# Kernel tuning notes

Hardware: AMD Instinct MI355X
Metric: run time of the kernel (lower is better)

Reference implementation:

```python
import jax, jax.numpy as jnp
import numpy as np

D_MODEL = 1024
N_HEADS = 16
HEAD_DIM = D_MODEL // N_HEADS


def setup_inputs() -> dict:
    key = jax.random.key(0)
    ks = jax.random.split(key, 10)
    B, NQ, S = 8, 64, 4096
    inv = 1.0 / np.sqrt(D_MODEL)
    inp = {
        "queries": jax.random.normal(ks[0], (B, NQ, D_MODEL), dtype=jnp.float32),
        "context": jax.random.normal(ks[1], (B, S, D_MODEL), dtype=jnp.float32),
        "wq": jax.random.normal(ks[2], (D_MODEL, D_MODEL), dtype=jnp.float32) * inv,
        "bq": jnp.zeros((D_MODEL,), dtype=jnp.float32),
        "wk": jax.random.normal(ks[3], (D_MODEL, D_MODEL), dtype=jnp.float32) * inv,
        "bk": jnp.zeros((D_MODEL,), dtype=jnp.float32),
        "wv": jax.random.normal(ks[4], (D_MODEL, D_MODEL), dtype=jnp.float32) * inv,
        "bv": jnp.zeros((D_MODEL,), dtype=jnp.float32),
        "wo": jax.random.normal(ks[5], (D_MODEL, D_MODEL), dtype=jnp.float32) * inv,
        "bo": jnp.zeros((D_MODEL,), dtype=jnp.float32),
    }
    return inp


def reference(queries, context, wq, bq, wk, bk, wv, bv, wo, bo):
    B, NQ, D = queries.shape
    S = context.shape[1]
    H, HD = N_HEADS, HEAD_DIM
    scale = HD ** -0.5
    # projections (x @ W^T + b, matching nn.Linear)
    q = queries @ wq.T + bq            # (B, NQ, D)
    k = context @ wk.T + bk            # (B, S, D)
    v = context @ wv.T + bv            # (B, S, D)
    q = q.reshape(B, NQ, H, HD).transpose(0, 2, 1, 3)  # (B, H, NQ, HD)
    k = k.reshape(B, S, H, HD).transpose(0, 2, 1, 3)   # (B, H, S, HD)
    v = v.reshape(B, S, H, HD).transpose(0, 2, 1, 3)   # (B, H, S, HD)
    attn = jnp.einsum('bhnd,bhsd->bhns', q, k) * scale
    attn = jax.nn.softmax(attn, axis=-1)
    # dropout is identity at eval / p=0
    out = jnp.einsum('bhns,bhsd->bhnd', attn, v)        # (B, H, NQ, HD)
    out = out.transpose(0, 2, 1, 3).reshape(B, NQ, D)   # (B, NQ, D)
    return out @ wo.T + bo
```

## Files before the change

kernel.cpp:

```cpp
#include <hip/hip_runtime.h>
#include <stdint.h>

#define BATCH   8
#define NQL     64
#define SLEN    4096
#define DMODEL  1024
#define NHEADS  16
#define HDIM    64

typedef float          f32x4  __attribute__((ext_vector_type(4)));
typedef __bf16         bf16x8 __attribute__((ext_vector_type(8)));
typedef unsigned int   u32x4  __attribute__((ext_vector_type(4)));
typedef unsigned short u16x4  __attribute__((ext_vector_type(4)));
typedef unsigned short u16x8  __attribute__((ext_vector_type(8)));

__device__ __forceinline__ unsigned short f2bf(float f) {
  unsigned int u = __builtin_bit_cast(unsigned int, f);
  u += 0x7FFFu + ((u >> 16) & 1u);
  return (unsigned short)(u >> 16);
}

__device__ __forceinline__ f32x4 mfma16(bf16x8 a, bf16x8 b, f32x4 c) {
  return __builtin_amdgcn_mfma_f32_16x16x32_bf16(a, b, c, 0, 0, 0);
}

__device__ __forceinline__ bf16x8 lds_frag(const char* p) {
  u32x4 v = *(const u32x4*)p;
  return __builtin_bit_cast(bf16x8, v);
}

__device__ __forceinline__ void gload_lds16(const void* g, void* l) {
  __builtin_amdgcn_global_load_lds((const __attribute__((address_space(1))) void*)g,
                                   (__attribute__((address_space(3))) void*)l, 16, 0, 0);
}

__global__ __launch_bounds__(256) void cvt_bf16_kernel(const float* __restrict__ in,
                                                       unsigned short* __restrict__ out,
                                                       int n8) {
  int i = blockIdx.x * 256 + threadIdx.x;
  if (i >= n8) return;
  const float4* p = (const float4*)in + (size_t)i * 2;
  float4 a = p[0], b = p[1];
  u16x8 o;
  o[0] = f2bf(a.x); o[1] = f2bf(a.y); o[2] = f2bf(a.z); o[3] = f2bf(a.w);
  o[4] = f2bf(b.x); o[5] = f2bf(b.y); o[6] = f2bf(b.z); o[7] = f2bf(b.w);
  *((u16x8*)out + i) = o;
}

template<int MODE>
__global__ __launch_bounds__(256)
void gemm_bt(const unsigned short* __restrict__ A, const unsigned short* __restrict__ Bw,
             const float* __restrict__ bias, void* __restrict__ Cout,
             int M, int N, int K) {
  __shared__ char lds[32768];
  char* ldsA = lds;
  char* ldsB = lds + 16384;

  const int tid  = threadIdx.x;
  const int wave = tid >> 6, lane = tid & 63;
  const int g    = lane >> 4, ln = lane & 15;
  const int nbn  = N >> 7;
  const int brow = (int)(blockIdx.x / nbn) << 7;
  const int bcol = (int)(blockIdx.x % nbn) << 7;
  const int wr   = wave >> 1, wc = wave & 1;

  f32x4 acc[4][4];
#pragma unroll
  for (int i = 0; i < 4; ++i)
#pragma unroll
    for (int j = 0; j < 4; ++j) acc[i][j] = (f32x4){0.f, 0.f, 0.f, 0.f};

  const int KT = K >> 6;
  const int srow = lane >> 3;
  const int srcs = (lane & 7) ^ (srow & 7);

  for (int kt = 0; kt < KT; ++kt) {
#pragma unroll
    for (int c = wave; c < 16; c += 4) {
      int row = (c << 3) + srow;
      const char* ga = (const char*)A + (((size_t)(brow + row) * K + (kt << 6) + (srcs << 3)) << 1);
      gload_lds16(ga, ldsA + (c << 10));
      const char* gb = (const char*)Bw + (((size_t)(bcol + row) * K + (kt << 6) + (srcs << 3)) << 1);
      gload_lds16(gb, ldsB + (c << 10));
    }
    asm volatile("s_waitcnt vmcnt(0)" ::: "memory");
    __syncthreads();

#pragma unroll
    for (int ks = 0; ks < 2; ++ks) {
      bf16x8 af[4], bfr[4];
      const int slot = ((ks << 2) + g) ^ (ln & 7);
#pragma unroll
      for (int mt = 0; mt < 4; ++mt) {
        int row = wr * 64 + mt * 16 + ln;
        af[mt] = lds_frag(ldsA + row * 128 + (slot << 4));
      }
#pragma unroll
      for (int nt = 0; nt < 4; ++nt) {
        int row = wc * 64 + nt * 16 + ln;
        bfr[nt] = lds_frag(ldsB + row * 128 + (slot << 4));
      }
#pragma unroll
      for (int mt = 0; mt < 4; ++mt)
#pragma unroll
        for (int nt = 0; nt < 4; ++nt)
          acc[mt][nt] = mfma16(af[mt], bfr[nt], acc[mt][nt]);
    }
    __syncthreads();
  }

#pragma unroll
  for (int mt = 0; mt < 4; ++mt) {
#pragma unroll
    for (int nt = 0; nt < 4; ++nt) {
      f32x4 v = acc[mt][nt];
      int r0 = brow + wr * 64 + mt * 16 + g * 4;
      int c  = bcol + wc * 64 + nt * 16 + ln;
      float bi = bias[c];
      if constexpr (MODE == 0) {
        unsigned short* Cb = (unsigned short*)Cout;
#pragma unroll
        for (int j = 0; j < 4; ++j) Cb[(size_t)(r0 + j) * N + c] = f2bf(v[j] + bi);
      } else if constexpr (MODE == 1) {
        float* Cf = (float*)Cout;
#pragma unroll
        for (int j = 0; j < 4; ++j) Cf[(size_t)(r0 + j) * N + c] = v[j] + bi;
      } else {
        u16x4 pk;
#pragma unroll
        for (int j = 0; j < 4; ++j) pk[j] = f2bf(v[j] + bi);
        size_t base = ((size_t)(r0 >> 12) * 1024 + c) * 4096 + (size_t)(r0 & 4095);
        *(u16x4*)((unsigned short*)Cout + base) = pk;
      }
    }
  }
}

__global__ __launch_bounds__(256)
void attn_kernel(const unsigned short* __restrict__ Qp,
                 const unsigned short* __restrict__ Kp,
                 const unsigned short* __restrict__ Vt,
                 unsigned short* __restrict__ Aout) {
  __shared__ char ldsKV[2][16384];
  __shared__ unsigned int plds[4 * 16 * 36];

  const int bh = blockIdx.x;
  const int b = bh >> 4, h = bh & 15;
  const int tid = threadIdx.x;
  const int wave = tid >> 6, lane = tid & 63;
  const int g = lane >> 4, ln = lane & 15;
  const int pbase = wave * 576 + ln * 36;
  const int srow = lane >> 3;
  const int srcs = (lane & 7) ^ (srow & 7);

  const unsigned short* qb =
      Qp + ((size_t)(b * 64 + wave * 16 + ln) * 1024) + h * 64 + g * 8;
  bf16x8 qf[2];
  qf[0] = __builtin_bit_cast(bf16x8, *(const u32x4*)qb);
  qf[1] = __builtin_bit_cast(bf16x8, *(const u32x4*)(qb + 32));

  f32x4 oacc[4];
#pragma unroll
  for (int i = 0; i < 4; ++i) oacc[i] = (f32x4){0.f, 0.f, 0.f, 0.f};
  float mrun = -1e30f, lrun = 0.f;

  auto stage = [&](int t, int buf) {
    int s0 = t << 6;
    char* bK = ldsKV[buf];
#pragma unroll
    for (int c4 = 0; c4 < 4; ++c4) {
      int c = wave * 4 + c4;
      int cc = c & 7;
      int row = (cc << 3) + srow;
      const char* gsrc;
      if (c < 8)
        gsrc = (const char*)Kp + (((size_t)((b << 12) + s0 + row) * 1024 + (h << 6) + (srcs << 3)) << 1);
      else
        gsrc = (const char*)Vt + (((size_t)((b << 10) + (h << 6) + row) * 4096 + s0 + (srcs << 3)) << 1);
      gload_lds16(gsrc, bK + ((c < 8) ? 0 : 8192) + (cc << 10));
    }
  };

  stage(0, 0);
  const int NT = SLEN / 64;
  for (int t = 0; t < NT; ++t) {
    asm volatile("s_waitcnt vmcnt(0)" ::: "memory");
    __syncthreads();
    if (t + 1 < NT) stage(t + 1, (t + 1) & 1);

    char* bufK = ldsKV[t & 1];
    char* bufV = bufK + 8192;

    f32x4 s4[4];
#pragma unroll
    for (int i = 0; i < 4; ++i) s4[i] = (f32x4){0.f, 0.f, 0.f, 0.f};
#pragma unroll
    for (int ks = 0; ks < 2; ++ks) {
      const int slot = ((ks << 2) + g) ^ (ln & 7);
#pragma unroll
      for (int mt = 0; mt < 4; ++mt) {
        int row = mt * 16 + ln;
        s4[mt] = mfma16(lds_frag(bufK + row * 128 + (slot << 4)), qf[ks], s4[mt]);
      }
    }

    float tmax = -1e30f;
#pragma unroll
    for (int mt = 0; mt < 4; ++mt)
#pragma unroll
      for (int j = 0; j < 4; ++j) {
        float sv = s4[mt][j] * 0.125f;
        s4[mt][j] = sv;
        tmax = fmaxf(tmax, sv);
      }
    tmax = fmaxf(tmax, __shfl_xor(tmax, 16));
    tmax = fmaxf(tmax, __shfl_xor(tmax, 32));
    float mnew = fmaxf(mrun, tmax);
    float factor = __expf(mrun - mnew);
    float psum = 0.f;
#pragma unroll
    for (int mt = 0; mt < 4; ++mt) {
      float p0 = __expf(s4[mt][0] - mnew);
      float p1 = __expf(s4[mt][1] - mnew);
      float p2 = __expf(s4[mt][2] - mnew);
      float p3 = __expf(s4[mt][3] - mnew);
      psum += (p0 + p1) + (p2 + p3);
      plds[pbase + mt * 8 + g * 2 + 0] = (unsigned)f2bf(p0) | ((unsigned)f2bf(p1) << 16);
      plds[pbase + mt * 8 + g * 2 + 1] = (unsigned)f2bf(p2) | ((unsigned)f2bf(p3) << 16);
    }
    psum += __shfl_xor(psum, 16);
    psum += __shfl_xor(psum, 32);
    lrun = lrun * factor + psum;
    mrun = mnew;

    float fj0 = __shfl(factor, g * 4 + 0);
    float fj1 = __shfl(factor, g * 4 + 1);
    float fj2 = __shfl(factor, g * 4 + 2);
    float fj3 = __shfl(factor, g * 4 + 3);
#pragma unroll
    for (int nt = 0; nt < 4; ++nt) {
      oacc[nt][0] *= fj0; oacc[nt][1] *= fj1; oacc[nt][2] *= fj2; oacc[nt][3] *= fj3;
    }

#pragma unroll
    for (int kt2 = 0; kt2 < 2; ++kt2) {
      u32x4 pv;
      int pidx = pbase + kt2 * 16 + g * 4;
      pv[0] = plds[pidx]; pv[1] = plds[pidx + 1]; pv[2] = plds[pidx + 2]; pv[3] = plds[pidx + 3];
      bf16x8 pa = __builtin_bit_cast(bf16x8, pv);
      const int slot = ((kt2 << 2) + g) ^ (ln & 7);
#pragma unroll
      for (int nt = 0; nt < 4; ++nt) {
        int row = nt * 16 + ln;
        oacc[nt] = mfma16(pa, lds_frag(bufV + row * 128 + (slot << 4)), oacc[nt]);
      }
    }
  }

  float l0 = __shfl(lrun, g * 4 + 0);
  float l1 = __shfl(lrun, g * 4 + 1);
  float l2 = __shfl(lrun, g * 4 + 2);
  float l3 = __shfl(lrun, g * 4 + 3);
  float r0 = 1.f / l0, r1 = 1.f / l1, r2 = 1.f / l2, r3 = 1.f / l3;
#pragma unroll
  for (int nt = 0; nt < 4; ++nt) {
    int col = h * 64 + nt * 16 + ln;
    size_t rbase = (size_t)(b * 64 + wave * 16 + g * 4) * 1024 + col;
    Aout[rbase + 0 * 1024] = f2bf(oacc[nt][0] * r0);
    Aout[rbase + 1 * 1024] = f2bf(oacc[nt][1] * r1);
    Aout[rbase + 2 * 1024] = f2bf(oacc[nt][2] * r2);
    Aout[rbase + 3 * 1024] = f2bf(oacc[nt][3] * r3);
  }
}

extern "C" void kernel_launch(void* const* d_in, const int* in_sizes, int n_in,
                              void* d_out, int out_size, void* d_ws, size_t ws_size,
                              hipStream_t stream) {
  const float* queries = (const float*)d_in[0];
  const float* context = (const float*)d_in[1];
  const float* wq = (const float*)d_in[2];
  const float* bq = (const float*)d_in[3];
  const float* wk = (const float*)d_in[4];
  const float* bk = (const float*)d_in[5];
  const float* wv = (const float*)d_in[6];
  const float* bv = (const float*)d_in[7];
  const float* wo = (const float*)d_in[8];
  const float* bo = (const float*)d_in[9];

  const size_t CTX_E = (size_t)BATCH * SLEN * DMODEL;
  const size_t QRY_E = (size_t)BATCH * NQL * DMODEL;
  const size_t W_E   = (size_t)DMODEL * DMODEL;

  char* ws = (char*)d_ws;
  size_t off = 0;
  auto alloc = [&](size_t bytes) {
    char* p = ws + off;
    off += (bytes + 255) & ~(size_t)255;
    return p;
  };
  unsigned short* ctx_bf = (unsigned short*)alloc(CTX_E * 2);
  unsigned short* q_bf   = (unsigned short*)alloc(QRY_E * 2);
  unsigned short* wq_bf  = (unsigned short*)alloc(W_E * 2);
  unsigned short* wk_bf  = (unsigned short*)alloc(W_E * 2);
  unsigned short* wv_bf  = (unsigned short*)alloc(W_E * 2);
  unsigned short* wo_bf  = (unsigned short*)alloc(W_E * 2);
  unsigned short* Qp     = (unsigned short*)alloc(QRY_E * 2);
  unsigned short* Kp     = (unsigned short*)alloc(CTX_E * 2);
  unsigned short* Vt     = (unsigned short*)alloc(CTX_E * 2);
  unsigned short* Ao     = (unsigned short*)alloc(QRY_E * 2);
  if (off > ws_size) return;

  cvt_bf16_kernel<<<dim3((int)(CTX_E / 8 / 256)), 256, 0, stream>>>(context, ctx_bf, (int)(CTX_E / 8));
  cvt_bf16_kernel<<<dim3((int)(QRY_E / 8 / 256)), 256, 0, stream>>>(queries, q_bf, (int)(QRY_E / 8));
  cvt_bf16_kernel<<<dim3((int)(W_E / 8 / 256)), 256, 0, stream>>>(wq, wq_bf, (int)(W_E / 8));
  cvt_bf16_kernel<<<dim3((int)(W_E / 8 / 256)), 256, 0, stream>>>(wk, wk_bf, (int)(W_E / 8));
  cvt_bf16_kernel<<<dim3((int)(W_E / 8 / 256)), 256, 0, stream>>>(wv, wv_bf, (int)(W_E / 8));
  cvt_bf16_kernel<<<dim3((int)(W_E / 8 / 256)), 256, 0, stream>>>(wo, wo_bf, (int)(W_E / 8));

  const int M_KV = BATCH * SLEN;
  const int M_Q  = BATCH * NQL;

  gemm_bt<0><<<dim3((M_KV / 128) * (DMODEL / 128)), 256, 0, stream>>>(ctx_bf, wk_bf, bk, Kp, M_KV, DMODEL, DMODEL);
  gemm_bt<2><<<dim3((M_KV / 128) * (DMODEL / 128)), 256, 0, stream>>>(ctx_bf, wv_bf, bv, Vt, M_KV, DMODEL, DMODEL);
  gemm_bt<0><<<dim3((M_Q / 128) * (DMODEL / 128)), 256, 0, stream>>>(q_bf, wq_bf, bq, Qp, M_Q, DMODEL, DMODEL);

  attn_kernel<<<dim3(BATCH * NHEADS), 256, 0, stream>>>(Qp, Kp, Vt, Ao);

  gemm_bt<1><<<dim3((M_Q / 128) * (DMODEL / 128)), 256, 0, stream>>>(Ao, wo_bf, bo, d_out, M_Q, DMODEL, DMODEL);
}
```

Measured before the change: 532.1 us.

## Split attention over sequence, double-buffer GEMM, fuse conversions, remap GEMM blocks

The sequence dimension of attention is split into 8 chunks, giving 1024 workgroups instead of 128, and a new combine kernel merges the partial softmax results. The GEMM moves from single-buffered to double-buffered LDS with a partial vmcnt wait and raises MFMA priority with s_setprio. It also remaps workgroup IDs across 8 XCDs. The six fp32-to-bf16 conversion launches are fused into one. This adds a combine launch plus extra fp32 partial-result traffic, and the partials reuse the ctx_bf buffer after the K/V GEMMs have finished with it.

```diff
diff --git a/kernel.cpp b/kernel.cpp
--- a/kernel.cpp
+++ b/kernel.cpp
@@ -7,6 +7,7 @@
 #define DMODEL  1024
 #define NHEADS  16
 #define HDIM    64
+#define NSPLIT  8
 
 typedef float          f32x4  __attribute__((ext_vector_type(4)));
 typedef __bf16         bf16x8 __attribute__((ext_vector_type(8)));
@@ -34,17 +35,27 @@
                                    (__attribute__((address_space(3))) void*)l, 16, 0, 0);
 }
 
-__global__ __launch_bounds__(256) void cvt_bf16_kernel(const float* __restrict__ in,
-                                                       unsigned short* __restrict__ out,
-                                                       int n8) {
+__global__ __launch_bounds__(256)
+void cvt6_kernel(const float* __restrict__ p0, const float* __restrict__ p1,
+                 const float* __restrict__ p2, const float* __restrict__ p3,
+                 const float* __restrict__ p4, const float* __restrict__ p5,
+                 unsigned short* __restrict__ o0, unsigned short* __restrict__ o1,
+                 unsigned short* __restrict__ o2, unsigned short* __restrict__ o3,
+                 unsigned short* __restrict__ o4, unsigned short* __restrict__ o5) {
   int i = blockIdx.x * 256 + threadIdx.x;
-  if (i >= n8) return;
-  const float4* p = (const float4*)in + (size_t)i * 2;
+  const float* src; unsigned short* dst; int rel;
+  if      (i < 4194304) { src = p0; dst = o0; rel = i; }
+  else if (i < 4259840) { src = p1; dst = o1; rel = i - 4194304; }
+  else if (i < 4390912) { src = p2; dst = o2; rel = i - 4259840; }
+  else if (i < 4521984) { src = p3; dst = o3; rel = i - 4390912; }
+  else if (i < 4653056) { src = p4; dst = o4; rel = i - 4521984; }
+  else                  { src = p5; dst = o5; rel = i - 4653056; }
+  const float4* p = (const float4*)src + (size_t)rel * 2;
   float4 a = p[0], b = p[1];
   u16x8 o;
   o[0] = f2bf(a.x); o[1] = f2bf(a.y); o[2] = f2bf(a.z); o[3] = f2bf(a.w);
   o[4] = f2bf(b.x); o[5] = f2bf(b.y); o[6] = f2bf(b.z); o[7] = f2bf(b.w);
-  *((u16x8*)out + i) = o;
+  *((u16x8*)dst + rel) = o;
 }
 
 template<int MODE>
@@ -52,16 +63,19 @@
 void gemm_bt(const unsigned short* __restrict__ A, const unsigned short* __restrict__ Bw,
              const float* __restrict__ bias, void* __restrict__ Cout,
              int M, int N, int K) {
-  __shared__ char lds[32768];
-  char* ldsA = lds;
-  char* ldsB = lds + 16384;
+  __shared__ char lds[65536];
 
   const int tid  = threadIdx.x;
   const int wave = tid >> 6, lane = tid & 63;
   const int g    = lane >> 4, ln = lane & 15;
+
+  const int nwg = (int)gridDim.x;
+  const int cpx = nwg >> 3;
+  const int bid = (int)blockIdx.x;
+  const int wg  = (bid & 7) * cpx + (bid >> 3);
   const int nbn  = N >> 7;
-  const int brow = (int)(blockIdx.x / nbn) << 7;
-  const int bcol = (int)(blockIdx.x % nbn) << 7;
+  const int brow = (wg / nbn) << 7;
+  const int bcol = (wg % nbn) << 7;
   const int wr   = wave >> 1, wc = wave & 1;
 
   f32x4 acc[4][4];
@@ -74,17 +88,28 @@
   const int srow = lane >> 3;
   const int srcs = (lane & 7) ^ (srow & 7);
 
-  for (int kt = 0; kt < KT; ++kt) {
+  auto stage = [&](int kt, char* buf) {
 #pragma unroll
     for (int c = wave; c < 16; c += 4) {
       int row = (c << 3) + srow;
       const char* ga = (const char*)A + (((size_t)(brow + row) * K + (kt << 6) + (srcs << 3)) << 1);
-      gload_lds16(ga, ldsA + (c << 10));
+      gload_lds16(ga, buf + (c << 10));
       const char* gb = (const char*)Bw + (((size_t)(bcol + row) * K + (kt << 6) + (srcs << 3)) << 1);
-      gload_lds16(gb, ldsB + (c << 10));
-    }
-    asm volatile("s_waitcnt vmcnt(0)" ::: "memory");
-    __syncthreads();
+      gload_lds16(gb, buf + 16384 + (c << 10));
+    }
+  };
+
+  stage(0, lds);
+  for (int kt = 0; kt < KT; ++kt) {
+    char* cur = lds + ((kt & 1) << 15);
+    if (kt + 1 < KT) {
+      stage(kt + 1, lds + (((kt + 1) & 1) << 15));
+      asm volatile("s_waitcnt vmcnt(8)" ::: "memory");
+    } else {
+      asm volatile("s_waitcnt vmcnt(0)" ::: "memory");
+    }
+    __builtin_amdgcn_s_barrier();
+    __builtin_amdgcn_sched_barrier(0);
 
 #pragma unroll
     for (int ks = 0; ks < 2; ++ks) {
@@ -93,20 +118,22 @@
 #pragma unroll
       for (int mt = 0; mt < 4; ++mt) {
         int row = wr * 64 + mt * 16 + ln;
-        af[mt] = lds_frag(ldsA + row * 128 + (slot << 4));
+        af[mt] = lds_frag(cur + row * 128 + (slot << 4));
       }
 #pragma unroll
       for (int nt = 0; nt < 4; ++nt) {
         int row = wc * 64 + nt * 16 + ln;
-        bfr[nt] = lds_frag(ldsB + row * 128 + (slot << 4));
-      }
+        bfr[nt] = lds_frag(cur + 16384 + row * 128 + (slot << 4));
+      }
+      __builtin_amdgcn_s_setprio(1);
 #pragma unroll
       for (int mt = 0; mt < 4; ++mt)
 #pragma unroll
         for (int nt = 0; nt < 4; ++nt)
           acc[mt][nt] = mfma16(af[mt], bfr[nt], acc[mt][nt]);
-    }
-    __syncthreads();
+      __builtin_amdgcn_s_setprio(0);
+    }
+    __builtin_amdgcn_s_barrier();
   }
 
 #pragma unroll
@@ -137,14 +164,17 @@
 }
 
 __global__ __launch_bounds__(256)
-void attn_kernel(const unsigned short* __restrict__ Qp,
-                 const unsigned short* __restrict__ Kp,
-                 const unsigned short* __restrict__ Vt,
-                 unsigned short* __restrict__ Aout) {
+void attn_split(const unsigned short* __restrict__ Qp,
+                const unsigned short* __restrict__ Kp,
+                const unsigned short* __restrict__ Vt,
+                float* __restrict__ Opart,
+                float* __restrict__ Mpart,
+                float* __restrict__ Lpart) {
   __shared__ char ldsKV[2][16384];
   __shared__ unsigned int plds[4 * 16 * 36];
 
-  const int bh = blockIdx.x;
+  const int bh = (int)blockIdx.x / NSPLIT;
+  const int sp = (int)blockIdx.x % NSPLIT;
   const int b = bh >> 4, h = bh & 15;
   const int tid = threadIdx.x;
   const int wave = tid >> 6, lane = tid & 63;
@@ -181,19 +211,21 @@
     }
   };
 
-  stage(0, 0);
-  const int NT = SLEN / 64;
-  for (int t = 0; t < NT; ++t) {
+  const int T0 = sp * (SLEN / 64 / NSPLIT);
+  const int NTL = SLEN / 64 / NSPLIT;
+  stage(T0, 0);
+  for (int tl = 0; tl < NTL; ++tl) {
     asm volatile("s_waitcnt vmcnt(0)" ::: "memory");
     __syncthreads();
-    if (t + 1 < NT) stage(t + 1, (t + 1) & 1);
-
-    char* bufK = ldsKV[t & 1];
+    if (tl + 1 < NTL) stage(T0 + tl + 1, (tl + 1) & 1);
+
+    char* bufK = ldsKV[tl & 1];
     char* bufV = bufK + 8192;
 
     f32x4 s4[4];
 #pragma unroll
     for (int i = 0; i < 4; ++i) s4[i] = (f32x4){0.f, 0.f, 0.f, 0.f};
+    __builtin_amdgcn_s_setprio(1);
 #pragma unroll
     for (int ks = 0; ks < 2; ++ks) {
       const int slot = ((ks << 2) + g) ^ (ln & 7);
@@ -203,6 +235,7 @@
         s4[mt] = mfma16(lds_frag(bufK + row * 128 + (slot << 4)), qf[ks], s4[mt]);
       }
     }
+    __builtin_amdgcn_s_setprio(0);
 
     float tmax = -1e30f;
 #pragma unroll
@@ -242,6 +275,7 @@
       oacc[nt][0] *= fj0; oacc[nt][1] *= fj1; oacc[nt][2] *= fj2; oacc[nt][3] *= fj3;
     }
 
+    __builtin_amdgcn_s_setprio(1);
 #pragma unroll
     for (int kt2 = 0; kt2 < 2; ++kt2) {
       u32x4 pv;
@@ -255,22 +289,49 @@
         oacc[nt] = mfma16(pa, lds_frag(bufV + row * 128 + (slot << 4)), oacc[nt]);
       }
     }
-  }
-
-  float l0 = __shfl(lrun, g * 4 + 0);
-  float l1 = __shfl(lrun, g * 4 + 1);
-  float l2 = __shfl(lrun, g * 4 + 2);
-  float l3 = __shfl(lrun, g * 4 + 3);
-  float r0 = 1.f / l0, r1 = 1.f / l1, r2 = 1.f / l2, r3 = 1.f / l3;
+    __builtin_amdgcn_s_setprio(0);
+  }
+
+  const int rowb = sp * (BATCH * NHEADS * 64) + bh * 64;
 #pragma unroll
   for (int nt = 0; nt < 4; ++nt) {
-    int col = h * 64 + nt * 16 + ln;
-    size_t rbase = (size_t)(b * 64 + wave * 16 + g * 4) * 1024 + col;
-    Aout[rbase + 0 * 1024] = f2bf(oacc[nt][0] * r0);
-    Aout[rbase + 1 * 1024] = f2bf(oacc[nt][1] * r1);
-    Aout[rbase + 2 * 1024] = f2bf(oacc[nt][2] * r2);
-    Aout[rbase + 3 * 1024] = f2bf(oacc[nt][3] * r3);
-  }
+#pragma unroll
+    for (int j = 0; j < 4; ++j) {
+      int q = wave * 16 + g * 4 + j;
+      Opart[(size_t)(rowb + q) * 64 + nt * 16 + ln] = oacc[nt][j];
+    }
+  }
+  if (g == 0) {
+    Mpart[rowb + wave * 16 + ln] = mrun;
+    Lpart[rowb + wave * 16 + ln] = lrun;
+  }
+}
+
+__global__ __launch_bounds__(256)
+void attn_combine(const float* __restrict__ Opart, const float* __restrict__ Mpart,
+                  const float* __restrict__ Lpart, unsigned short* __restrict__ Aout) {
+  const int blk = blockIdx.x;
+  const int bh = blk >> 4;
+  const int q  = ((blk & 15) << 2) + (threadIdx.x >> 6);
+  const int hd = threadIdx.x & 63;
+  const int row = bh * 64 + q;
+
+  float mi[NSPLIT];
+  float M = -1e30f;
+#pragma unroll
+  for (int i = 0; i < NSPLIT; ++i) {
+    mi[i] = Mpart[i * 8192 + row];
+    M = fmaxf(M, mi[i]);
+  }
+  float L = 0.f, o = 0.f;
+#pragma unroll
+  for (int i = 0; i < NSPLIT; ++i) {
+    float w = __expf(mi[i] - M);
+    L += Lpart[i * 8192 + row] * w;
+    o += Opart[(size_t)(i * 8192 + row) * 64 + hd] * w;
+  }
+  const int b = bh >> 4, h = bh & 15;
+  Aout[(size_t)(b * 64 + q) * 1024 + h * 64 + hd] = f2bf(o / L);
 }
 
 extern "C" void kernel_launch(void* const* d_in, const int* in_sizes, int n_in,
@@ -310,21 +371,23 @@
   unsigned short* Ao     = (unsigned short*)alloc(QRY_E * 2);
   if (off > ws_size) return;
 
-  cvt_bf16_kernel<<<dim3((int)(CTX_E / 8 / 256)), 256, 0, stream>>>(context, ctx_bf, (int)(CTX_E / 8));
-  cvt_bf16_kernel<<<dim3((int)(QRY_E / 8 / 256)), 256, 0, stream>>>(queries, q_bf, (int)(QRY_E / 8));
-  cvt_bf16_kernel<<<dim3((int)(W_E / 8 / 256)), 256, 0, stream>>>(wq, wq_bf, (int)(W_E / 8));
-  cvt_bf16_kernel<<<dim3((int)(W_E / 8 / 256)), 256, 0, stream>>>(wk, wk_bf, (int)(W_E / 8));
-  cvt_bf16_kernel<<<dim3((int)(W_E / 8 / 256)), 256, 0, stream>>>(wv, wv_bf, (int)(W_E / 8));
-  cvt_bf16_kernel<<<dim3((int)(W_E / 8 / 256)), 256, 0, stream>>>(wo, wo_bf, (int)(W_E / 8));
+  float* Opart = (float*)ctx_bf;
+  float* Mpart = Opart + (size_t)NSPLIT * BATCH * NHEADS * 64 * 64;
+  float* Lpart = Mpart + (size_t)NSPLIT * BATCH * NHEADS * 64;
+
+  cvt6_kernel<<<dim3(18688), 256, 0, stream>>>(context, queries, wq, wk, wv, wo,
+                                               ctx_bf, q_bf, wq_bf, wk_bf, wv_bf, wo_bf);
 
   const int M_KV = BATCH * SLEN;
   const int M_Q  = BATCH * NQL;
 
   gemm_bt<0><<<dim3((M_KV / 128) * (DMODEL / 128)), 256, 0, stream>>>(ctx_bf, wk_bf, bk, Kp, M_KV, DMODEL, DMODEL);
   gemm_bt<2><<<dim3((M_KV / 128) * (DMODEL / 128)), 256, 0, stream>>>(ctx_bf, wv_bf, bv, Vt, M_KV, DMODEL, DMODEL);
+
   gemm_bt<0><<<dim3((M_Q / 128) * (DMODEL / 128)), 256, 0, stream>>>(q_bf, wq_bf, bq, Qp, M_Q, DMODEL, DMODEL);
 
-  attn_kernel<<<dim3(BATCH * NHEADS), 256, 0, stream>>>(Qp, Kp, Vt, Ao);
+  attn_split<<<dim3(BATCH * NHEADS * NSPLIT), 256, 0, stream>>>(Qp, Kp, Vt, Opart, Mpart, Lpart);
+  attn_combine<<<dim3(BATCH * NHEADS * 16), 256, 0, stream>>>(Opart, Mpart, Lpart, Ao);
 
   gemm_bt<1><<<dim3((M_Q / 128) * (DMODEL / 128)), 256, 0, stream>>>(Ao, wo_bf, bo, d_out, M_Q, DMODEL, DMODEL);
 }
```

Result: faster. 435.7 us (-18.1%).
